# Kernel tuning notes

Measured on AMD Instinct MI355X. Metric: run time of the kernel, lower is better.

Reference implementation:

```python
import jax, jax.numpy as jnp
import numpy as np

NUM_HEADS = 16

def setup_inputs() -> dict:
    key = jax.random.key(0)
    ks = jax.random.split(key, 7)
    B, N, C, R = 2, 2048, 1024, 64
    s = lambda fan_in: 1.0 / np.sqrt(fan_in)
    return {
        "x": jax.random.normal(ks[0], (B, N, C), dtype=jnp.float32),
        "w_qkv_a": jax.random.uniform(ks[1], (C, R), jnp.float32, -s(C), s(C)),
        "w_qkv_b": jax.random.uniform(ks[2], (R, 3 * C), jnp.float32, -s(R), s(R)),
        "w_proj_a": jax.random.uniform(ks[3], (C, R), jnp.float32, -s(C), s(C)),
        "b_proj_a": jax.random.uniform(ks[4], (R,), jnp.float32, -s(C), s(C)),
        "w_proj_b": jax.random.uniform(ks[5], (R, C), jnp.float32, -s(R), s(R)),
        "b_proj_b": jax.random.uniform(ks[6], (C,), jnp.float32, -s(R), s(R)),
    }

def reference(x, w_qkv_a, w_qkv_b, w_proj_a, b_proj_a, w_proj_b, b_proj_b):
    B, N, C = x.shape
    H = NUM_HEADS
    Dh = C // H
    scale = Dh ** -0.5
    # LoRA QKV: dim -> rank -> 3*dim with exact GELU between (no bias, qkv_bias=False)
    qkv = jax.nn.gelu(x @ w_qkv_a, approximate=False) @ w_qkv_b  # [B,N,3C]
    qkv = qkv.reshape(B, N, 3, H, Dh).transpose(2, 0, 3, 1, 4)  # [3,B,H,N,Dh]
    q, k, v = qkv[0] * scale, qkv[1], qkv[2]
    attn = jax.nn.softmax(jnp.einsum("bhqd,bhkd->bhqk", q, k), axis=-1)
    out = jnp.einsum("bhqk,bhkd->bhqd", attn, v)  # [B,H,N,Dh]
    out = out.transpose(0, 2, 1, 3).reshape(B, N, C)
    # LoRA proj: dim -> rank -> dim with bias (proj_bias=True)
    out = jax.nn.gelu(out @ w_proj_a + b_proj_a, approximate=False) @ w_proj_b + b_proj_b
    return out
```

## Files before the change

### kernel.cpp

```cpp
#include <hip/hip_runtime.h>
#include <cstdint>
#include <cstddef>


typedef short short8 __attribute__((ext_vector_type(8)));
typedef float f32x4 __attribute__((ext_vector_type(4)));
typedef __fp16 half2v __attribute__((ext_vector_type(2)));
typedef __fp16 half4 __attribute__((ext_vector_type(4)));

#define MFMA16(a, b, c) __builtin_amdgcn_mfma_f32_16x16x32_bf16((a), (b), (c), 0, 0, 0)
#define MFMA16F(a, b, c) __builtin_amdgcn_mfma_f32_16x16x16f16((a), (b), (c), 0, 0, 0)

#define QSCALE 0.18033688011112042f

__device__ __forceinline__ float fexp2(float x) { return __builtin_amdgcn_exp2f(x); }

__device__ __forceinline__ uint16_t f2b(float f) {
    return (uint16_t)((__float_as_uint(f) + 0x8000u) >> 16);
}
__device__ __forceinline__ uint32_t pkbf(float a, float b) {
    uint32_t ua = __float_as_uint(a) + 0x8000u;
    uint32_t ub = __float_as_uint(b) + 0x8000u;
    return __builtin_amdgcn_perm(ub, ua, 0x07060302);
}
__device__ __forceinline__ uint16_t f2h(float f) {
    half2v t = __builtin_amdgcn_cvt_pkrtz(f, f);
    return __builtin_bit_cast(uint16_t, t[0]);
}
__device__ __forceinline__ float gelu_exact(float x) {
    return 0.5f * x * (1.0f + erff(x * 0.70710678118654752440f));
}
__device__ __forceinline__ short8 ld8(const uint16_t* p) {
    return *reinterpret_cast<const short8*>(p);
}

__global__ __launch_bounds__(256) void prep(const float* __restrict__ x,
                                            const float* __restrict__ wqa,
                                            const float* __restrict__ wqb,
                                            const float* __restrict__ wpa,
                                            const float* __restrict__ wpb,
                                            uint16_t* __restrict__ xb,
                                            uint16_t* __restrict__ wqaT,
                                            uint16_t* __restrict__ wqbT,
                                            uint16_t* __restrict__ wpaT,
                                            uint16_t* __restrict__ wpbT) {
    const int bid = blockIdx.x;
    if (bid < 2048) {
        size_t i = ((size_t)bid * 256 + threadIdx.x) * 8;
        f32x4 a0 = *reinterpret_cast<const f32x4*>(x + i);
        f32x4 a1 = *reinterpret_cast<const f32x4*>(x + i + 4);
        uint32_t* o = reinterpret_cast<uint32_t*>(xb + i);
        o[0] = pkbf(a0[0], a0[1]);
        o[1] = pkbf(a0[2], a0[3]);
        o[2] = pkbf(a1[0], a1[1]);
        o[3] = pkbf(a1[2], a1[3]);
        return;
    }
    int i = (bid - 2048) * 256 + threadIdx.x;
    if (i < 65536) {
        int r = i >> 6, c = i & 63;
        wqaT[(size_t)c * 1024 + r] = f2b(wqa[i]);
    } else if (i < 262144) {
        int j = i - 65536;
        int r = j / 3072, c = j - r * 3072;
        wqbT[(size_t)c * 64 + r] = f2b(wqb[j]);
    } else if (i < 327680) {
        int j = i - 262144;
        int r = j >> 6, c = j & 63;
        wpaT[(size_t)c * 1024 + r] = f2b(wpa[j]);
    } else {
        int j = i - 327680;
        int r = j >> 10, c = j & 1023;
        wpbT[(size_t)c * 64 + r] = f2b(wpb[j]);
    }
}

__global__ __launch_bounds__(512) void rank_gemm(const uint16_t* __restrict__ X,
                                                 const uint16_t* __restrict__ WT,
                                                 uint16_t* __restrict__ out) {
    __shared__ float ps[4][16][17];
    const int tid = threadIdx.x;
    const int wave = tid >> 6, lane = tid & 63;
    const int l16 = lane & 15, quad = lane >> 4;
    const int cc = wave & 3, kh = wave >> 2;
    const int rowg = blockIdx.x;

    const uint16_t* ap = X + (size_t)(rowg * 16 + l16) * 1024 + kh * 512 + quad * 8;
    const uint16_t* bp = WT + (size_t)(cc * 16 + l16) * 1024 + kh * 512 + quad * 8;

    f32x4 acc = {0.f, 0.f, 0.f, 0.f};
#pragma unroll 8
    for (int k = 0; k < 16; ++k) {
        acc = MFMA16(ld8(ap + k * 32), ld8(bp + k * 32), acc);
    }

    if (kh == 1) {
#pragma unroll
        for (int r = 0; r < 4; ++r) ps[cc][quad * 4 + r][l16] = acc[r];
    }
    __syncthreads();
    if (kh == 0) {
        const int col = cc * 16 + l16;
#pragma unroll
        for (int r = 0; r < 4; ++r) {
            int row = rowg * 16 + quad * 4 + r;
            float v = acc[r] + ps[cc][quad * 4 + r][l16];
            out[(size_t)row * 64 + col] = f2b(gelu_exact(v));
        }
    }
}

__global__ __launch_bounds__(256) void expand_qkv(const uint16_t* __restrict__ H1,
                                                  const uint16_t* __restrict__ WT,
                                                  uint16_t* __restrict__ Qb,
                                                  uint16_t* __restrict__ Kf,
                                                  uint16_t* __restrict__ Vf) {
    __shared__ __align__(16) uint16_t tl[64 * 72];
    const int tid = threadIdx.x;
    const int wave = tid >> 6;
    const int lane = tid & 63;
    const int l16 = lane & 15, quad = lane >> 4;
    const int colg = blockIdx.x % 48;
    const int rowblk = blockIdx.x / 48;
    const int rowg = rowblk * 4 + wave;

    const uint16_t* ap = H1 + (size_t)(rowg * 16 + l16) * 64 + quad * 8;
    const uint16_t* bp = WT + ((size_t)colg * 64 + l16) * 64 + quad * 8;

    const int which = colg >> 4;
    const int h = colg & 15;
    const int b = rowblk >> 5;
    const int tt = rowblk & 31;
    const int bh = b * 16 + h;

    f32x4 acc[4];
#pragma unroll
    for (int c = 0; c < 4; ++c) acc[c] = (f32x4){0.f, 0.f, 0.f, 0.f};

    if (which < 2) {
#pragma unroll
        for (int i = 0; i < 2; ++i) {
            short8 a = ld8(ap + i * 32);
#pragma unroll
            for (int c = 0; c < 4; ++c) {
                acc[c] = MFMA16(a, ld8(bp + (size_t)c * 1024 + i * 32), acc[c]);
            }
        }
        const float sc = (which == 0) ? QSCALE : 1.0f;
#pragma unroll
        for (int c = 0; c < 4; ++c) {
#pragma unroll
            for (int r = 0; r < 4; ++r) {
                tl[(wave * 16 + quad * 4 + r) * 72 + c * 16 + l16] = f2b(acc[c][r] * sc);
            }
        }
        __syncthreads();
        if (which == 0) {
            const int nl = tid >> 2, d0 = (tid & 3) * 16;
            const int n = rowblk * 64 + nl;
            uint16_t* dst = Qb + ((size_t)bh * 2048 + (n & 2047)) * 64 + d0;
            *reinterpret_cast<short8*>(dst) = ld8(&tl[nl * 72 + d0]);
            *reinterpret_cast<short8*>(dst + 8) = ld8(&tl[nl * 72 + d0 + 8]);
        } else {
            const int kc = tid >> 7, h2 = (tid >> 6) & 1;
            const int qd = (tid >> 4) & 3, lk = tid & 15;
            const int key = kc * 16 + lk;
            const int d0 = h2 * 32 + qd * 8;
            uint16_t* dst = Kf + ((size_t)bh * 32 + tt) * 4096 + (size_t)tid * 8;
            *reinterpret_cast<short8*>(dst) = ld8(&tl[key * 72 + d0]);
            *reinterpret_cast<short8*>(dst + 2048) = ld8(&tl[(key + 32) * 72 + d0]);
        }
    } else {
#pragma unroll
        for (int i = 0; i < 2; ++i) {
            short8 a = ld8(ap + i * 32);
#pragma unroll
            for (int c = 0; c < 4; ++c) {
                acc[c] = MFMA16(ld8(bp + (size_t)c * 1024 + i * 32), a, acc[c]);
            }
        }
#pragma unroll
        for (int c = 0; c < 4; ++c) {
#pragma unroll
            for (int r = 0; r < 4; ++r) {
                tl[(c * 16 + quad * 4 + r) * 72 + wave * 16 + l16] = f2h(acc[c][r]);
            }
        }
        __syncthreads();
        const int dc = tid >> 7, kp = (tid >> 6) & 1;
        const int qk = (tid >> 4) & 3, ld16 = tid & 15;
        const int d = dc * 16 + ld16;
        const int k0 = kp * 32 + qk * 4;
        uint16_t* dst = Vf + ((size_t)bh * 32 + tt) * 4096 + (size_t)tid * 8;
        union { short8 s; uint64_t u[2]; } pk;
        pk.u[0] = *reinterpret_cast<const uint64_t*>(&tl[d * 72 + k0]);
        pk.u[1] = *reinterpret_cast<const uint64_t*>(&tl[d * 72 + k0 + 16]);
        *reinterpret_cast<short8*>(dst) = pk.s;
        pk.u[0] = *reinterpret_cast<const uint64_t*>(&tl[(d + 32) * 72 + k0]);
        pk.u[1] = *reinterpret_cast<const uint64_t*>(&tl[(d + 32) * 72 + k0 + 16]);
        *reinterpret_cast<short8*>(dst + 2048) = pk.s;
    }
}

__global__ __launch_bounds__(256) void attn_kernel(const uint16_t* __restrict__ Qb,
                                                   const uint16_t* __restrict__ Kf,
                                                   const uint16_t* __restrict__ Vf,
                                                   uint16_t* __restrict__ AO) {
    __shared__ __align__(16) uint16_t kt[4096];
    __shared__ __align__(16) uint16_t vt[4096];
    __shared__ __align__(16) uint16_t pws[128 * 72];

    const int tid = threadIdx.x;
    const int wave = tid >> 6;
    const int lane = tid & 63;
    const int l16 = lane & 15, quad = lane >> 4;
    const int bh = blockIdx.x >> 4;
    const int qc = blockIdx.x & 15;
    const int qbase = qc * 128 + wave * 32;

    short8 qf[2][2];
#pragma unroll
    for (int g = 0; g < 2; ++g) {
        const uint16_t* qp = Qb + ((size_t)bh * 2048 + qbase + g * 16 + l16) * 64 + quad * 8;
        qf[g][0] = ld8(qp);
        qf[g][1] = ld8(qp + 32);
    }

    f32x4 ot[2][4];
    float lp[2] = {0.f, 0.f};
#pragma unroll
    for (int g = 0; g < 2; ++g)
#pragma unroll
        for (int dc = 0; dc < 4; ++dc) ot[g][dc] = (f32x4){0.f, 0.f, 0.f, 0.f};

    for (int t = 0; t < 32; ++t) {
        __syncthreads();
        {
            const uint16_t* kg = Kf + ((size_t)bh * 32 + t) * 4096 + tid * 8;
            *reinterpret_cast<short8*>(&kt[tid * 8]) = ld8(kg);
            *reinterpret_cast<short8*>(&kt[2048 + tid * 8]) = ld8(kg + 2048);
            const uint16_t* vg = Vf + ((size_t)bh * 32 + t) * 4096 + tid * 8;
            *reinterpret_cast<short8*>(&vt[tid * 8]) = ld8(vg);
            *reinterpret_cast<short8*>(&vt[2048 + tid * 8]) = ld8(vg + 2048);
        }
        __syncthreads();

        half4 pb[2][4];
#pragma unroll
        for (int kc = 0; kc < 4; ++kc) {
            const short8 a0 = ld8(&kt[kc * 1024 + lane * 8]);
            const short8 a1 = ld8(&kt[kc * 1024 + 512 + lane * 8]);
#pragma unroll
            for (int g = 0; g < 2; ++g) {
                f32x4 st = {0.f, 0.f, 0.f, 0.f};
                st = MFMA16(a0, qf[g][0], st);
                st = MFMA16(a1, qf[g][1], st);
                float p0 = fexp2(st[0]), p1 = fexp2(st[1]);
                float p2 = fexp2(st[2]), p3 = fexp2(st[3]);
                lp[g] += (p0 + p1) + (p2 + p3);
                half2v lo = __builtin_amdgcn_cvt_pkrtz(p0, p1);
                half2v hi = __builtin_amdgcn_cvt_pkrtz(p2, p3);
                pb[g][kc] = __builtin_shufflevector(lo, hi, 0, 1, 2, 3);
            }
        }

#pragma unroll
        for (int dc = 0; dc < 4; ++dc) {
#pragma unroll
            for (int kp = 0; kp < 2; ++kp) {
                union { short8 s; half4 h[2]; } vv;
                vv.s = ld8(&vt[dc * 1024 + kp * 512 + lane * 8]);
#pragma unroll
                for (int g = 0; g < 2; ++g) {
                    ot[g][dc] = MFMA16F(vv.h[0], pb[g][kp * 2], ot[g][dc]);
                    ot[g][dc] = MFMA16F(vv.h[1], pb[g][kp * 2 + 1], ot[g][dc]);
                }
            }
        }
    }

#pragma unroll
    for (int g = 0; g < 2; ++g) {
        float ls = lp[g];
        ls += __shfl_xor(ls, 16, 64);
        ls += __shfl_xor(ls, 32, 64);
        const float inv = 1.0f / ls;
        uint16_t* pw = &pws[(wave * 32 + g * 16 + l16) * 72];
#pragma unroll
        for (int dc = 0; dc < 4; ++dc) {
            uint32_t* w = reinterpret_cast<uint32_t*>(&pw[dc * 16 + quad * 4]);
            w[0] = pkbf(ot[g][dc][0] * inv, ot[g][dc][1] * inv);
            w[1] = pkbf(ot[g][dc][2] * inv, ot[g][dc][3] * inv);
        }
    }
    __syncthreads();

    const int b = bh >> 4, h = bh & 15;
    const int ql = tid >> 1, d0 = (tid & 1) * 32;
    const int grow = b * 2048 + qc * 128 + ql;
    uint16_t* dst = AO + (size_t)grow * 1024 + h * 64 + d0;
    const uint16_t* src = &pws[ql * 72 + d0];
    *reinterpret_cast<short8*>(dst) = ld8(src);
    *reinterpret_cast<short8*>(dst + 8) = ld8(src + 8);
    *reinterpret_cast<short8*>(dst + 16) = ld8(src + 16);
    *reinterpret_cast<short8*>(dst + 24) = ld8(src + 24);
}

__global__ __launch_bounds__(512) void proj_fused(const uint16_t* __restrict__ AO,
                                                  const uint16_t* __restrict__ wpaT,
                                                  const float* __restrict__ bpa,
                                                  const uint16_t* __restrict__ wpbT,
                                                  const float* __restrict__ bpb,
                                                  float* __restrict__ out) {
    __shared__ float ps[4][16][17];
    __shared__ __align__(16) uint16_t h2L[16 * 72];
    const int tid = threadIdx.x;
    const int wave = tid >> 6, lane = tid & 63;
    const int l16 = lane & 15, quad = lane >> 4;
    const int cc = wave & 3, kh = wave >> 2;
    const int rowg = blockIdx.x;

    {
        const uint16_t* ap = AO + (size_t)(rowg * 16 + l16) * 1024 + kh * 512 + quad * 8;
        const uint16_t* bp = wpaT + (size_t)(cc * 16 + l16) * 1024 + kh * 512 + quad * 8;
        f32x4 acc = {0.f, 0.f, 0.f, 0.f};
#pragma unroll 8
        for (int k = 0; k < 16; ++k) {
            acc = MFMA16(ld8(ap + k * 32), ld8(bp + k * 32), acc);
        }
        if (kh == 1) {
#pragma unroll
            for (int r = 0; r < 4; ++r) ps[cc][quad * 4 + r][l16] = acc[r];
        }
        __syncthreads();
        if (kh == 0) {
            const int col = cc * 16 + l16;
            const float bv = bpa[col];
#pragma unroll
            for (int r = 0; r < 4; ++r) {
                float v = acc[r] + ps[cc][quad * 4 + r][l16] + bv;
                h2L[(quad * 4 + r) * 72 + col] = f2b(gelu_exact(v));
            }
        }
        __syncthreads();
    }

    const short8 a0 = ld8(&h2L[l16 * 72 + quad * 8]);
    const short8 a1 = ld8(&h2L[l16 * 72 + 32 + quad * 8]);
#pragma unroll
    for (int i = 0; i < 8; ++i) {
        const int col0 = (wave * 8 + i) * 16;
        const uint16_t* bp = wpbT + (size_t)(col0 + l16) * 64 + quad * 8;
        f32x4 acc = {0.f, 0.f, 0.f, 0.f};
        acc = MFMA16(a0, ld8(bp), acc);
        acc = MFMA16(a1, ld8(bp + 32), acc);
        const float bv = bpb[col0 + l16];
#pragma unroll
        for (int r = 0; r < 4; ++r) {
            int row = rowg * 16 + quad * 4 + r;
            out[(size_t)row * 1024 + col0 + l16] = acc[r] + bv;
        }
    }
}

extern "C" void kernel_launch(void* const* d_in, const int* in_sizes, int n_in,
                              void* d_out, int out_size, void* d_ws, size_t ws_size,
                              hipStream_t stream) {
    const float* x   = (const float*)d_in[0];
    const float* wqa = (const float*)d_in[1];
    const float* wqb = (const float*)d_in[2];
    const float* wpa = (const float*)d_in[3];
    const float* bpa = (const float*)d_in[4];
    const float* wpb = (const float*)d_in[5];
    const float* bpb = (const float*)d_in[6];
    float* out = (float*)d_out;
    uint16_t* ws = (uint16_t*)d_ws;

    uint16_t* wqaT = ws + 0;
    uint16_t* wqbT = ws + 65536;
    uint16_t* wpaT = ws + 262144;
    uint16_t* wpbT = ws + 327680;
    uint16_t* h1   = ws + 393216;
    uint16_t* Qb   = ws + 655360;
    uint16_t* Kf   = ws + 4849664;
    uint16_t* xb   = Kf;
    uint16_t* Vf   = ws + 9043968;
    uint16_t* AO   = ws + 13238272;
    (void)in_sizes; (void)n_in; (void)out_size; (void)ws_size;

    prep<<<3584, 256, 0, stream>>>(x, wqa, wqb, wpa, wpb, xb, wqaT, wqbT, wpaT, wpbT);
    rank_gemm<<<256, 512, 0, stream>>>(xb, wqaT, h1);
    expand_qkv<<<3072, 256, 0, stream>>>(h1, wqbT, Qb, Kf, Vf);
    attn_kernel<<<512, 256, 0, stream>>>(Qb, Kf, Vf, AO);
    proj_fused<<<256, 512, 0, stream>>>(AO, wpaT, bpa, wpbT, bpb, out);
}
```

Before: 172.0 us.

## Fuse x bf16 conversion into rank GEMM and double-buffer K/V tiles in attention

Removes the separate pass that converted x to bf16. The first rank GEMM now reads fp32 x directly and packs it to bf16 in registers, which saves a full write and read of the activation. The attention kernel now double-buffers K/V tiles in shared memory. It prefetches the next tile into registers during compute and stores it after, so only one barrier per iteration is needed instead of two. This roughly doubles the K/V shared-memory footprint, and the output staging buffer is aliased onto the same shared space, which raises register pressure.

```diff
diff --git a/kernel.cpp b/kernel.cpp
--- a/kernel.cpp
+++ b/kernel.cpp
@@ -33,30 +33,19 @@
 __device__ __forceinline__ short8 ld8(const uint16_t* p) {
     return *reinterpret_cast<const short8*>(p);
 }
-
-__global__ __launch_bounds__(256) void prep(const float* __restrict__ x,
-                                            const float* __restrict__ wqa,
-                                            const float* __restrict__ wqb,
-                                            const float* __restrict__ wpa,
-                                            const float* __restrict__ wpb,
-                                            uint16_t* __restrict__ xb,
-                                            uint16_t* __restrict__ wqaT,
-                                            uint16_t* __restrict__ wqbT,
-                                            uint16_t* __restrict__ wpaT,
-                                            uint16_t* __restrict__ wpbT) {
-    const int bid = blockIdx.x;
-    if (bid < 2048) {
-        size_t i = ((size_t)bid * 256 + threadIdx.x) * 8;
-        f32x4 a0 = *reinterpret_cast<const f32x4*>(x + i);
-        f32x4 a1 = *reinterpret_cast<const f32x4*>(x + i + 4);
-        uint32_t* o = reinterpret_cast<uint32_t*>(xb + i);
-        o[0] = pkbf(a0[0], a0[1]);
-        o[1] = pkbf(a0[2], a0[3]);
-        o[2] = pkbf(a1[0], a1[1]);
-        o[3] = pkbf(a1[2], a1[3]);
-        return;
-    }
-    int i = (bid - 2048) * 256 + threadIdx.x;
+__device__ __forceinline__ void st8(uint16_t* p, short8 v) {
+    *reinterpret_cast<short8*>(p) = v;
+}
+
+__global__ __launch_bounds__(256) void prep_w(const float* __restrict__ wqa,
+                                              const float* __restrict__ wqb,
+                                              const float* __restrict__ wpa,
+                                              const float* __restrict__ wpb,
+                                              uint16_t* __restrict__ wqaT,
+                                              uint16_t* __restrict__ wqbT,
+                                              uint16_t* __restrict__ wpaT,
+                                              uint16_t* __restrict__ wpbT) {
+    int i = blockIdx.x * 256 + threadIdx.x;
     if (i < 65536) {
         int r = i >> 6, c = i & 63;
         wqaT[(size_t)c * 1024 + r] = f2b(wqa[i]);
@@ -75,9 +64,9 @@
     }
 }
 
-__global__ __launch_bounds__(512) void rank_gemm(const uint16_t* __restrict__ X,
-                                                 const uint16_t* __restrict__ WT,
-                                                 uint16_t* __restrict__ out) {
+__global__ __launch_bounds__(512) void rank_gemm_f32(const float* __restrict__ X,
+                                                     const uint16_t* __restrict__ WT,
+                                                     uint16_t* __restrict__ out) {
     __shared__ float ps[4][16][17];
     const int tid = threadIdx.x;
     const int wave = tid >> 6, lane = tid & 63;
@@ -85,13 +74,20 @@
     const int cc = wave & 3, kh = wave >> 2;
     const int rowg = blockIdx.x;
 
-    const uint16_t* ap = X + (size_t)(rowg * 16 + l16) * 1024 + kh * 512 + quad * 8;
+    const float* ap = X + (size_t)(rowg * 16 + l16) * 1024 + kh * 512 + quad * 8;
     const uint16_t* bp = WT + (size_t)(cc * 16 + l16) * 1024 + kh * 512 + quad * 8;
 
     f32x4 acc = {0.f, 0.f, 0.f, 0.f};
 #pragma unroll 8
     for (int k = 0; k < 16; ++k) {
-        acc = MFMA16(ld8(ap + k * 32), ld8(bp + k * 32), acc);
+        f32x4 a0 = *reinterpret_cast<const f32x4*>(ap + k * 32);
+        f32x4 a1 = *reinterpret_cast<const f32x4*>(ap + k * 32 + 4);
+        union { short8 s; uint32_t u[4]; } af;
+        af.u[0] = pkbf(a0[0], a0[1]);
+        af.u[1] = pkbf(a0[2], a0[3]);
+        af.u[2] = pkbf(a1[0], a1[1]);
+        af.u[3] = pkbf(a1[2], a1[3]);
+        acc = MFMA16(af.s, ld8(bp + k * 32), acc);
     }
 
     if (kh == 1) {
@@ -159,16 +155,16 @@
             const int nl = tid >> 2, d0 = (tid & 3) * 16;
             const int n = rowblk * 64 + nl;
             uint16_t* dst = Qb + ((size_t)bh * 2048 + (n & 2047)) * 64 + d0;
-            *reinterpret_cast<short8*>(dst) = ld8(&tl[nl * 72 + d0]);
-            *reinterpret_cast<short8*>(dst + 8) = ld8(&tl[nl * 72 + d0 + 8]);
+            st8(dst, ld8(&tl[nl * 72 + d0]));
+            st8(dst + 8, ld8(&tl[nl * 72 + d0 + 8]));
         } else {
             const int kc = tid >> 7, h2 = (tid >> 6) & 1;
             const int qd = (tid >> 4) & 3, lk = tid & 15;
             const int key = kc * 16 + lk;
             const int d0 = h2 * 32 + qd * 8;
             uint16_t* dst = Kf + ((size_t)bh * 32 + tt) * 4096 + (size_t)tid * 8;
-            *reinterpret_cast<short8*>(dst) = ld8(&tl[key * 72 + d0]);
-            *reinterpret_cast<short8*>(dst + 2048) = ld8(&tl[(key + 32) * 72 + d0]);
+            st8(dst, ld8(&tl[key * 72 + d0]));
+            st8(dst + 2048, ld8(&tl[(key + 32) * 72 + d0]));
         }
     } else {
 #pragma unroll
@@ -195,10 +191,10 @@
         union { short8 s; uint64_t u[2]; } pk;
         pk.u[0] = *reinterpret_cast<const uint64_t*>(&tl[d * 72 + k0]);
         pk.u[1] = *reinterpret_cast<const uint64_t*>(&tl[d * 72 + k0 + 16]);
-        *reinterpret_cast<short8*>(dst) = pk.s;
+        st8(dst, pk.s);
         pk.u[0] = *reinterpret_cast<const uint64_t*>(&tl[(d + 32) * 72 + k0]);
         pk.u[1] = *reinterpret_cast<const uint64_t*>(&tl[(d + 32) * 72 + k0 + 16]);
-        *reinterpret_cast<short8*>(dst + 2048) = pk.s;
+        st8(dst + 2048, pk.s);
     }
 }
 
@@ -206,9 +202,7 @@
                                                    const uint16_t* __restrict__ Kf,
                                                    const uint16_t* __restrict__ Vf,
                                                    uint16_t* __restrict__ AO) {
-    __shared__ __align__(16) uint16_t kt[4096];
-    __shared__ __align__(16) uint16_t vt[4096];
-    __shared__ __align__(16) uint16_t pws[128 * 72];
+    __shared__ __align__(16) uint16_t smem[16384];
 
     const int tid = threadIdx.x;
     const int wave = tid >> 6;
@@ -233,17 +227,29 @@
 #pragma unroll
         for (int dc = 0; dc < 4; ++dc) ot[g][dc] = (f32x4){0.f, 0.f, 0.f, 0.f};
 
+    const uint16_t* kg = Kf + (size_t)bh * 32 * 4096 + tid * 8;
+    const uint16_t* vg = Vf + (size_t)bh * 32 * 4096 + tid * 8;
+
+    st8(&smem[tid * 8], ld8(kg));
+    st8(&smem[2048 + tid * 8], ld8(kg + 2048));
+    st8(&smem[8192 + tid * 8], ld8(vg));
+    st8(&smem[8192 + 2048 + tid * 8], ld8(vg + 2048));
+    __syncthreads();
+
     for (int t = 0; t < 32; ++t) {
-        __syncthreads();
-        {
-            const uint16_t* kg = Kf + ((size_t)bh * 32 + t) * 4096 + tid * 8;
-            *reinterpret_cast<short8*>(&kt[tid * 8]) = ld8(kg);
-            *reinterpret_cast<short8*>(&kt[2048 + tid * 8]) = ld8(kg + 2048);
-            const uint16_t* vg = Vf + ((size_t)bh * 32 + t) * 4096 + tid * 8;
-            *reinterpret_cast<short8*>(&vt[tid * 8]) = ld8(vg);
-            *reinterpret_cast<short8*>(&vt[2048 + tid * 8]) = ld8(vg + 2048);
-        }
-        __syncthreads();
+        const int cur = t & 1, nxt = cur ^ 1;
+        uint16_t* kt = &smem[cur * 4096];
+        uint16_t* vt = &smem[8192 + cur * 4096];
+
+        short8 pk0, pk1, pv0, pv1;
+        if (t + 1 < 32) {
+            const uint16_t* kg2 = kg + (size_t)(t + 1) * 4096;
+            const uint16_t* vg2 = vg + (size_t)(t + 1) * 4096;
+            pk0 = ld8(kg2);
+            pk1 = ld8(kg2 + 2048);
+            pv0 = ld8(vg2);
+            pv1 = ld8(vg2 + 2048);
+        }
 
         half4 pb[2][4];
 #pragma unroll
@@ -277,8 +283,17 @@
                 }
             }
         }
-    }
-
+
+        if (t + 1 < 32) {
+            st8(&smem[nxt * 4096 + tid * 8], pk0);
+            st8(&smem[nxt * 4096 + 2048 + tid * 8], pk1);
+            st8(&smem[8192 + nxt * 4096 + tid * 8], pv0);
+            st8(&smem[8192 + nxt * 4096 + 2048 + tid * 8], pv1);
+        }
+        __syncthreads();
+    }
+
+    uint16_t* pws = smem;
 #pragma unroll
     for (int g = 0; g < 2; ++g) {
         float ls = lp[g];
@@ -300,10 +315,10 @@
     const int grow = b * 2048 + qc * 128 + ql;
     uint16_t* dst = AO + (size_t)grow * 1024 + h * 64 + d0;
     const uint16_t* src = &pws[ql * 72 + d0];
-    *reinterpret_cast<short8*>(dst) = ld8(src);
-    *reinterpret_cast<short8*>(dst + 8) = ld8(src + 8);
-    *reinterpret_cast<short8*>(dst + 16) = ld8(src + 16);
-    *reinterpret_cast<short8*>(dst + 24) = ld8(src + 24);
+    st8(dst, ld8(src));
+    st8(dst + 8, ld8(src + 8));
+    st8(dst + 16, ld8(src + 16));
+    st8(dst + 24, ld8(src + 24));
 }
 
 __global__ __launch_bounds__(512) void proj_fused(const uint16_t* __restrict__ AO,
@@ -383,13 +398,12 @@
     uint16_t* h1   = ws + 393216;
     uint16_t* Qb   = ws + 655360;
     uint16_t* Kf   = ws + 4849664;
-    uint16_t* xb   = Kf;
     uint16_t* Vf   = ws + 9043968;
     uint16_t* AO   = ws + 13238272;
     (void)in_sizes; (void)n_in; (void)out_size; (void)ws_size;
 
-    prep<<<3584, 256, 0, stream>>>(x, wqa, wqb, wpa, wpb, xb, wqaT, wqbT, wpaT, wpbT);
-    rank_gemm<<<256, 512, 0, stream>>>(xb, wqaT, h1);
+    prep_w<<<1536, 256, 0, stream>>>(wqa, wqb, wpa, wpb, wqaT, wqbT, wpaT, wpbT);
+    rank_gemm_f32<<<256, 512, 0, stream>>>(x, wqaT, h1);
     expand_qkv<<<3072, 256, 0, stream>>>(h1, wqbT, Qb, Kf, Vf);
     attn_kernel<<<512, 256, 0, stream>>>(Qb, Kf, Vf, AO);
     proj_fused<<<256, 512, 0, stream>>>(AO, wpaT, bpa, wpbT, bpb, out);
```

Measured after the change: 178.4 us. 3.7% more time.
